# Kernel optimization log

Hardware: AMD Instinct MI355X
Metric: run time of the kernel (lower is better)

Reference implementation:

```python
import jax, jax.numpy as jnp
import numpy as np

B, CIN, H, W = 128, 64, 32, 32
COUT, K, STRIDE, PAD = 64, 3, 1, 1
HO = (H + 2 * PAD - K) // STRIDE + 1
WO = (W + 2 * PAD - K) // STRIDE + 1


def setup_inputs() -> dict:
    key = jax.random.key(0)
    k1, k2 = jax.random.split(key)
    x = jax.random.normal(k1, (B, CIN, H, W), dtype=jnp.float32)
    # weight scaled like torch init: randn / sqrt(k*k*Cin) (orthogonal_ in torch just
    # re-orthogonalizes; scale here matches the fan-in normalization)
    weight = jax.random.normal(k2, (HO, WO, COUT, CIN, K, K), dtype=jnp.float32) / np.sqrt(K * K * CIN)
    bias = jnp.full((COUT, HO, WO), 0.5, dtype=jnp.float32)
    return {"x": x, "weight": weight, "bias": bias}


def reference(x, weight, bias):
    # pad spatial dims
    xp = jnp.pad(x, ((0, 0), (0, 0), (PAD, PAD), (PAD, PAD)))
    # gather row windows: [B, C, Ho, K, Wp]
    ri = (jnp.arange(HO) * STRIDE)[:, None] + jnp.arange(K)[None, :]  # [Ho, K]
    ci = (jnp.arange(WO) * STRIDE)[:, None] + jnp.arange(K)[None, :]  # [Wo, K]
    rows = xp[:, :, ri, :]           # [B, C, Ho, K, Wp]
    patches = rows[:, :, :, :, ci]   # [B, C, Ho, K, Wo, K]
    # per-location matmul: b c h p w q , h w d c p q -> b d h w
    out = jnp.einsum('bchpwq,hwdcpq->bdhw', patches, weight)
    return out + bias[None]
```

## Files before the change

### kernel.cpp

```cpp
#include <hip/hip_runtime.h>
#include <hip/hip_bf16.h>

#define KT 576

typedef __attribute__((ext_vector_type(8))) short  short8;
typedef __attribute__((ext_vector_type(4))) float  f32x4;

#define VMCNT(n) asm volatile("s_waitcnt vmcnt(" #n ")" ::: "memory")
#define SB() __builtin_amdgcn_sched_barrier(0)

__device__ __forceinline__ unsigned short f2bf(float f) {
  union { float f; unsigned int u; } v; v.f = f;
  return (unsigned short)((v.u + 0x7FFFu + ((v.u >> 16) & 1u)) >> 16);
}

__global__ __launch_bounds__(256) void xC2_kernel(const float* __restrict__ x,
                                                  unsigned short* __restrict__ xC2) {
  const int hp = blockIdx.x, bb = blockIdx.y, t = threadIdx.x;
  __shared__ unsigned short tile[32 * 1024];
  const bool interior = (hp >= 1 && hp <= 32);
  if (interior) {
#pragma unroll 4
    for (int i = 0; i < 32; ++i) {
      const int row = i * 32 + (t >> 3);
      const int bl = row >> 6, c = row & 63;
      const int k = t & 7;
      const float4 v = *(const float4*)(x + ((size_t)(bb * 16 + bl) * 64 + c) * 1024 +
                                        (hp - 1) * 32 + k * 4);
      const int base = (k * 4) * 1024 + (c >> 3) * 128 + bl * 8 + (c & 7);
      tile[base]        = f2bf(v.x);
      tile[base + 1024] = f2bf(v.y);
      tile[base + 2048] = f2bf(v.z);
      tile[base + 3072] = f2bf(v.w);
    }
  }
  __syncthreads();
  unsigned short* dst = xC2 + (size_t)hp * 278528 + (size_t)bb * 1024;
  const uint4 z = make_uint4(0u, 0u, 0u, 0u);
  for (int idx = t; idx < 34 * 128; idx += 256) {
    const int wp = idx >> 7, s = idx & 127;
    uint4 v = z;
    if (interior && wp >= 1 && wp <= 32) v = *(const uint4*)&tile[(wp - 1) * 1024 + s * 8];
    *(uint4*)(dst + (size_t)wp * 8192 + s * 8) = v;
  }
}

__global__ __launch_bounds__(256, 1) void lc_main(const float* __restrict__ Wt,
                                                  const float* __restrict__ bias,
                                                  const unsigned short* __restrict__ xC2,
                                                  float* __restrict__ out) {
  __shared__ unsigned short Wl[2][32 * KT];
  __shared__ float blds[128];

  const int bid = (int)blockIdx.x;
  const int swz = (bid & 7) * 64 + (bid >> 3);
  const int h = swz >> 4, rem = swz & 15, wq = rem >> 1, half = rem & 1;
  const int t = threadIdx.x, lane = t & 63, wv = t >> 6;
  const int l15 = lane & 15, lg = lane >> 4;

  if (t < 128)
    blds[t] = bias[(half * 32 + (t & 31)) * 1024 + h * 32 + wq * 4 + (t >> 5)];

  const unsigned short* xA = xC2 + (size_t)wv * 2048 + lg * 128 + l15 * 8;
  const int x7 = l15 & 7;
  const int wrow0 = l15 * KT;
  const int wrow1 = (16 + l15) * KT;

  f32x4 acc[4][2][2];
#pragma unroll
  for (int j = 0; j < 4; ++j)
#pragma unroll
    for (int bt = 0; bt < 2; ++bt)
#pragma unroll
      for (int dt = 0; dt < 2; ++dt) acc[j][bt][dt] = (f32x4){0.f, 0.f, 0.f, 0.f};

  short8 As0[3][3], As1[3][3];
  float4 wreg[18];

#define ISSUE_W18(jj)                                                         \
  {                                                                           \
    const float* ws = Wt + (size_t)(h * 32 + wq * 4 + (jj)) * (64 * KT) +     \
                      (size_t)half * (32 * KT);                               \
    _Pragma("unroll")                                                         \
    for (int i = 0; i < 18; ++i) {                                            \
      const float4* p = (const float4*)ws + (i * 256 + t);                    \
      asm volatile("global_load_dwordx4 %0, %1, off" : "=v"(wreg[i]) : "v"(p)); \
    }                                                                         \
  }

#define ISSUE_W3(jj, ck)                                                      \
  {                                                                           \
    const float* ws = Wt + (size_t)(h * 32 + wq * 4 + (jj)) * (64 * KT) +     \
                      (size_t)half * (32 * KT);                               \
    _Pragma("unroll")                                                         \
    for (int i = 0; i < 3; ++i) {                                             \
      const float4* p = (const float4*)ws + (((ck) * 3 + i) * 256 + t);       \
      asm volatile("global_load_dwordx4 %0, %1, off" : "=v"(wreg[(ck) * 3 + i]) : "v"(p)); \
    }                                                                         \
  }

#define ISSUE_A(K)                                                            \
  {                                                                           \
    _Pragma("unroll")                                                         \
    for (int s = 0; s < 3; ++s) {                                             \
      const int step = ((K) % 6) * 3 + s;                                     \
      const int pq = step >> 1, p = pq / 3, q = pq - p * 3;                   \
      const size_t off = (size_t)(h + p) * 278528 +                           \
                         (size_t)(wq * 4 + (K) / 6 + q) * 8192 + (step & 1) * 512; \
      const short8* p0 = (const short8*)(xA + off);                           \
      const short8* p1 = (const short8*)(xA + off + 1024);                    \
      asm volatile("global_load_dwordx4 %0, %1, off" : "=v"(As0[(K) % 3][s]) : "v"(p0)); \
      asm volatile("global_load_dwordx4 %0, %1, off" : "=v"(As1[(K) % 3][s]) : "v"(p1)); \
    }                                                                         \
  }

#define SCATTER(buf)                                                          \
  {                                                                           \
    _Pragma("unroll")                                                         \
    for (int i = 0; i < 18; ++i) {                                            \
      const int f = (i * 256 + t) * 4;                                        \
      const int d = (((unsigned)(f >> 6)) * 7282u) >> 16;                     \
      int kn = f - d * 576;                                                   \
      int c = ((unsigned)kn * 7282u) >> 16;                                   \
      int r = kn - c * 9;                                                     \
      const float vv[4] = {wreg[i].x, wreg[i].y, wreg[i].z, wreg[i].w};       \
      _Pragma("unroll")                                                       \
      for (int jx = 0; jx < 4; ++jx) {                                        \
        const int kp = r * 64 + c;                                            \
        const int slot = (kp >> 3) ^ (d & 7);                                 \
        Wl[buf][d * KT + slot * 8 + (kp & 7)] = f2bf(vv[jx]);                 \
        if (++r == 9) { r = 0; ++c; }                                         \
      }                                                                       \
    }                                                                         \
  }

#define MFMAS(jj, gg)                                                         \
  {                                                                           \
    _Pragma("unroll")                                                         \
    for (int s = 0; s < 3; ++s) {                                             \
      const int sb = ((gg) * 3 + s) * 4 + lg;                                 \
      const short8 b0 = *(const short8*)&Wl[(jj) & 1][wrow0 + ((sb ^ x7) << 3)]; \
      const short8 b1 = *(const short8*)&Wl[(jj) & 1][wrow1 + ((sb ^ x7) << 3)]; \
      acc[(jj)][0][0] = __builtin_amdgcn_mfma_f32_16x16x32_bf16(As0[((jj) * 6 + (gg)) % 3][s], b0, acc[(jj)][0][0], 0, 0, 0); \
      acc[(jj)][1][0] = __builtin_amdgcn_mfma_f32_16x16x32_bf16(As1[((jj) * 6 + (gg)) % 3][s], b0, acc[(jj)][1][0], 0, 0, 0); \
      acc[(jj)][0][1] = __builtin_amdgcn_mfma_f32_16x16x32_bf16(As0[((jj) * 6 + (gg)) % 3][s], b1, acc[(jj)][0][1], 0, 0, 0); \
      acc[(jj)][1][1] = __builtin_amdgcn_mfma_f32_16x16x32_bf16(As1[((jj) * 6 + (gg)) % 3][s], b1, acc[(jj)][1][1], 0, 0, 0); \
    }                                                                         \
  }

#define STEP(jj, gg, NN) { VMCNT(NN); SB(); MFMAS(jj, gg) }
#define STEPNW(jj, gg)   { SB(); MFMAS(jj, gg) }

  ISSUE_W18(0);
  ISSUE_A(0); ISSUE_A(1); ISSUE_A(2);
  VMCNT(18); SB();
  SCATTER(0);
  __syncthreads(); SB();

  STEP(0, 0, 12); ISSUE_A(3); ISSUE_W3(1, 0);
  STEP(0, 1, 15); ISSUE_A(4); ISSUE_W3(1, 1);
  STEP(0, 2, 18); ISSUE_A(5); ISSUE_W3(1, 2);
  STEP(0, 3, 21); ISSUE_W3(1, 3); ISSUE_A(6);
  STEP(0, 4, 21); ISSUE_W3(1, 4); ISSUE_A(7);
  STEP(0, 5, 21); ISSUE_W3(1, 5); ISSUE_A(8);
  VMCNT(6); SB(); SCATTER(1);
  __syncthreads(); SB();

  STEPNW(1, 0);   ISSUE_A(9);  ISSUE_W3(2, 0);
  STEPNW(1, 1);   ISSUE_A(10); ISSUE_W3(2, 1);
  STEP(1, 2, 18); ISSUE_A(11); ISSUE_W3(2, 2);
  STEP(1, 3, 21); ISSUE_W3(2, 3); ISSUE_A(12);
  STEP(1, 4, 21); ISSUE_W3(2, 4); ISSUE_A(13);
  STEP(1, 5, 21); ISSUE_W3(2, 5); ISSUE_A(14);
  VMCNT(6); SB(); SCATTER(0);
  __syncthreads(); SB();

  STEPNW(2, 0);   ISSUE_A(15); ISSUE_W3(3, 0);
  STEPNW(2, 1);   ISSUE_A(16); ISSUE_W3(3, 1);
  STEP(2, 2, 18); ISSUE_A(17); ISSUE_W3(3, 2);
  STEP(2, 3, 21); ISSUE_W3(3, 3); ISSUE_A(18);
  STEP(2, 4, 21); ISSUE_W3(3, 4); ISSUE_A(19);
  STEP(2, 5, 21); ISSUE_W3(3, 5); ISSUE_A(20);
  VMCNT(6); SB(); SCATTER(1);
  __syncthreads(); SB();

  STEPNW(3, 0);   ISSUE_A(21);
  STEPNW(3, 1);   ISSUE_A(22);
  STEP(3, 2, 12); ISSUE_A(23);
  STEP(3, 3, 12);
  STEP(3, 4, 6);
  STEP(3, 5, 0);

#pragma unroll
  for (int dt = 0; dt < 2; ++dt) {
    const int dd = dt * 16 + l15;
    const int dg = half * 32 + dd;
    const float bv0 = blds[dd], bv1 = blds[32 + dd], bv2 = blds[64 + dd], bv3 = blds[96 + dd];
#pragma unroll
    for (int bt = 0; bt < 2; ++bt) {
#pragma unroll
      for (int i = 0; i < 4; ++i) {
        const int b = wv * 32 + bt * 16 + lg * 4 + i;
        float4 v;
        v.x = acc[0][bt][dt][i] + bv0;
        v.y = acc[1][bt][dt][i] + bv1;
        v.z = acc[2][bt][dt][i] + bv2;
        v.w = acc[3][bt][dt][i] + bv3;
        *(float4*)(out + (size_t)b * 65536 + (size_t)dg * 1024 + h * 32 + wq * 4) = v;
      }
    }
  }
}

extern "C" void kernel_launch(void* const* d_in, const int* in_sizes, int n_in,
                              void* d_out, int out_size, void* d_ws, size_t ws_size,
                              hipStream_t stream) {
  const float* x    = (const float*)d_in[0];
  const float* wt   = (const float*)d_in[1];
  const float* bias = (const float*)d_in[2];
  float* out        = (float*)d_out;
  unsigned short* xC2 = (unsigned short*)d_ws;

  xC2_kernel<<<dim3(34, 8), 256, 0, stream>>>(x, xC2);
  lc_main<<<512, 256, 0, stream>>>(wt, bias, xC2, out);
}
```

Before: 70.37 us.

## Shrink weight staging registers and A prefetch depth to cut VGPR pressure

Replaces the 18-register weight staging buffer with a 6-register one, scattering weights into LDS in three chunks interleaved with the MFMA steps. The A prefetch ring shrinks from three slots to two. The pipeline is rescheduled through a PHASE macro with new vmcnt waits. The goal is to lower VGPR usage, allowing more occupancy or avoiding spills. The cost is shallower prefetch depth and more frequent waits, which can expose global-load latency.

```diff
diff --git a/kernel.cpp b/kernel.cpp
--- a/kernel.cpp
+++ b/kernel.cpp
@@ -74,28 +74,17 @@
 #pragma unroll
       for (int dt = 0; dt < 2; ++dt) acc[j][bt][dt] = (f32x4){0.f, 0.f, 0.f, 0.f};
 
-  short8 As0[3][3], As1[3][3];
-  float4 wreg[18];
-
-#define ISSUE_W18(jj)                                                         \
+  short8 As0[2][3], As1[2][3];
+  float4 wreg[6];
+
+#define ISSUE_W6(jj, bb)                                                      \
   {                                                                           \
     const float* ws = Wt + (size_t)(h * 32 + wq * 4 + (jj)) * (64 * KT) +     \
                       (size_t)half * (32 * KT);                               \
     _Pragma("unroll")                                                         \
-    for (int i = 0; i < 18; ++i) {                                            \
-      const float4* p = (const float4*)ws + (i * 256 + t);                    \
+    for (int i = 0; i < 6; ++i) {                                             \
+      const float4* p = (const float4*)ws + (((bb) * 6 + i) * 256 + t);       \
       asm volatile("global_load_dwordx4 %0, %1, off" : "=v"(wreg[i]) : "v"(p)); \
-    }                                                                         \
-  }
-
-#define ISSUE_W3(jj, ck)                                                      \
-  {                                                                           \
-    const float* ws = Wt + (size_t)(h * 32 + wq * 4 + (jj)) * (64 * KT) +     \
-                      (size_t)half * (32 * KT);                               \
-    _Pragma("unroll")                                                         \
-    for (int i = 0; i < 3; ++i) {                                             \
-      const float4* p = (const float4*)ws + (((ck) * 3 + i) * 256 + t);       \
-      asm volatile("global_load_dwordx4 %0, %1, off" : "=v"(wreg[(ck) * 3 + i]) : "v"(p)); \
     }                                                                         \
   }
 
@@ -109,16 +98,16 @@
                          (size_t)(wq * 4 + (K) / 6 + q) * 8192 + (step & 1) * 512; \
       const short8* p0 = (const short8*)(xA + off);                           \
       const short8* p1 = (const short8*)(xA + off + 1024);                    \
-      asm volatile("global_load_dwordx4 %0, %1, off" : "=v"(As0[(K) % 3][s]) : "v"(p0)); \
-      asm volatile("global_load_dwordx4 %0, %1, off" : "=v"(As1[(K) % 3][s]) : "v"(p1)); \
-    }                                                                         \
-  }
-
-#define SCATTER(buf)                                                          \
-  {                                                                           \
-    _Pragma("unroll")                                                         \
-    for (int i = 0; i < 18; ++i) {                                            \
-      const int f = (i * 256 + t) * 4;                                        \
+      asm volatile("global_load_dwordx4 %0, %1, off" : "=v"(As0[(K) % 2][s]) : "v"(p0)); \
+      asm volatile("global_load_dwordx4 %0, %1, off" : "=v"(As1[(K) % 2][s]) : "v"(p1)); \
+    }                                                                         \
+  }
+
+#define SCATTER6(buf, bb)                                                     \
+  {                                                                           \
+    _Pragma("unroll")                                                         \
+    for (int i = 0; i < 6; ++i) {                                             \
+      const int f = ((((bb) * 6) + i) * 256 + t) * 4;                         \
       const int d = (((unsigned)(f >> 6)) * 7282u) >> 16;                     \
       int kn = f - d * 576;                                                   \
       int c = ((unsigned)kn * 7282u) >> 16;                                   \
@@ -141,53 +130,41 @@
       const int sb = ((gg) * 3 + s) * 4 + lg;                                 \
       const short8 b0 = *(const short8*)&Wl[(jj) & 1][wrow0 + ((sb ^ x7) << 3)]; \
       const short8 b1 = *(const short8*)&Wl[(jj) & 1][wrow1 + ((sb ^ x7) << 3)]; \
-      acc[(jj)][0][0] = __builtin_amdgcn_mfma_f32_16x16x32_bf16(As0[((jj) * 6 + (gg)) % 3][s], b0, acc[(jj)][0][0], 0, 0, 0); \
-      acc[(jj)][1][0] = __builtin_amdgcn_mfma_f32_16x16x32_bf16(As1[((jj) * 6 + (gg)) % 3][s], b0, acc[(jj)][1][0], 0, 0, 0); \
-      acc[(jj)][0][1] = __builtin_amdgcn_mfma_f32_16x16x32_bf16(As0[((jj) * 6 + (gg)) % 3][s], b1, acc[(jj)][0][1], 0, 0, 0); \
-      acc[(jj)][1][1] = __builtin_amdgcn_mfma_f32_16x16x32_bf16(As1[((jj) * 6 + (gg)) % 3][s], b1, acc[(jj)][1][1], 0, 0, 0); \
+      acc[(jj)][0][0] = __builtin_amdgcn_mfma_f32_16x16x32_bf16(As0[((jj) * 6 + (gg)) % 2][s], b0, acc[(jj)][0][0], 0, 0, 0); \
+      acc[(jj)][1][0] = __builtin_amdgcn_mfma_f32_16x16x32_bf16(As1[((jj) * 6 + (gg)) % 2][s], b0, acc[(jj)][1][0], 0, 0, 0); \
+      acc[(jj)][0][1] = __builtin_amdgcn_mfma_f32_16x16x32_bf16(As0[((jj) * 6 + (gg)) % 2][s], b1, acc[(jj)][0][1], 0, 0, 0); \
+      acc[(jj)][1][1] = __builtin_amdgcn_mfma_f32_16x16x32_bf16(As1[((jj) * 6 + (gg)) % 2][s], b1, acc[(jj)][1][1], 0, 0, 0); \
     }                                                                         \
   }
 
 #define STEP(jj, gg, NN) { VMCNT(NN); SB(); MFMAS(jj, gg) }
-#define STEPNW(jj, gg)   { SB(); MFMAS(jj, gg) }
-
-  ISSUE_W18(0);
-  ISSUE_A(0); ISSUE_A(1); ISSUE_A(2);
-  VMCNT(18); SB();
-  SCATTER(0);
+
+#define PHASE(jj)                                                             \
+  STEP(jj, 0, 6);  ISSUE_A(6 * (jj) + 2); ISSUE_W6((jj) + 1, 0);              \
+  STEP(jj, 1, 12); ISSUE_A(6 * (jj) + 3);                                     \
+  STEP(jj, 2, 12); ISSUE_A(6 * (jj) + 4);                                     \
+    VMCNT(12); SB(); SCATTER6(((jj) + 1) & 1, 0); ISSUE_W6((jj) + 1, 1);      \
+  STEP(jj, 3, 12); ISSUE_A(6 * (jj) + 5);                                     \
+  STEP(jj, 4, 12); ISSUE_A(6 * (jj) + 6);                                     \
+    VMCNT(12); SB(); SCATTER6(((jj) + 1) & 1, 1); ISSUE_W6((jj) + 1, 2);      \
+  STEP(jj, 5, 12); ISSUE_A(6 * (jj) + 7);                                     \
+    VMCNT(6); SB(); SCATTER6(((jj) + 1) & 1, 2);                              \
   __syncthreads(); SB();
 
-  STEP(0, 0, 12); ISSUE_A(3); ISSUE_W3(1, 0);
-  STEP(0, 1, 15); ISSUE_A(4); ISSUE_W3(1, 1);
-  STEP(0, 2, 18); ISSUE_A(5); ISSUE_W3(1, 2);
-  STEP(0, 3, 21); ISSUE_W3(1, 3); ISSUE_A(6);
-  STEP(0, 4, 21); ISSUE_W3(1, 4); ISSUE_A(7);
-  STEP(0, 5, 21); ISSUE_W3(1, 5); ISSUE_A(8);
-  VMCNT(6); SB(); SCATTER(1);
+  ISSUE_W6(0, 0); ISSUE_A(0); ISSUE_A(1);
+  VMCNT(12); SB(); SCATTER6(0, 0); ISSUE_W6(0, 1);
+  VMCNT(0);  SB(); SCATTER6(0, 1); ISSUE_W6(0, 2);
+  VMCNT(0);  SB(); SCATTER6(0, 2);
   __syncthreads(); SB();
 
-  STEPNW(1, 0);   ISSUE_A(9);  ISSUE_W3(2, 0);
-  STEPNW(1, 1);   ISSUE_A(10); ISSUE_W3(2, 1);
-  STEP(1, 2, 18); ISSUE_A(11); ISSUE_W3(2, 2);
-  STEP(1, 3, 21); ISSUE_W3(2, 3); ISSUE_A(12);
-  STEP(1, 4, 21); ISSUE_W3(2, 4); ISSUE_A(13);
-  STEP(1, 5, 21); ISSUE_W3(2, 5); ISSUE_A(14);
-  VMCNT(6); SB(); SCATTER(0);
-  __syncthreads(); SB();
-
-  STEPNW(2, 0);   ISSUE_A(15); ISSUE_W3(3, 0);
-  STEPNW(2, 1);   ISSUE_A(16); ISSUE_W3(3, 1);
-  STEP(2, 2, 18); ISSUE_A(17); ISSUE_W3(3, 2);
-  STEP(2, 3, 21); ISSUE_W3(3, 3); ISSUE_A(18);
-  STEP(2, 4, 21); ISSUE_W3(3, 4); ISSUE_A(19);
-  STEP(2, 5, 21); ISSUE_W3(3, 5); ISSUE_A(20);
-  VMCNT(6); SB(); SCATTER(1);
-  __syncthreads(); SB();
-
-  STEPNW(3, 0);   ISSUE_A(21);
-  STEPNW(3, 1);   ISSUE_A(22);
-  STEP(3, 2, 12); ISSUE_A(23);
-  STEP(3, 3, 12);
+  PHASE(0)
+  PHASE(1)
+  PHASE(2)
+
+  STEP(3, 0, 6);  ISSUE_A(20);
+  STEP(3, 1, 6);  ISSUE_A(21);
+  STEP(3, 2, 6);  ISSUE_A(22);
+  STEP(3, 3, 6);  ISSUE_A(23);
   STEP(3, 4, 6);
   STEP(3, 5, 0);
 
```

After: 62.76 us. 10.8% less time.
